# Optimization experiments

Hardware: AMD Instinct MI355X
Metric: run time of the kernel (lower is better)

Reference implementation:

```python
import math
import jax, jax.numpy as jnp
import numpy as np

B, T, D = 2048, 50, 256
NEG = -100000.0

def setup_inputs() -> dict:
    key = jax.random.key(0)
    ks = jax.random.split(key, 9)
    return {
        "x": jax.random.normal(ks[0], (B, T, D), dtype=jnp.float32),
        "mask": jax.random.randint(ks[1], (B, T, 1), 0, 2, dtype=jnp.int32),
        "time_decay": jax.random.uniform(ks[2], (B, T, 1), dtype=jnp.float32),
        "Wq": jax.random.normal(ks[3], (D, D), dtype=jnp.float32) * (1.0 / math.sqrt(D)),
        "bq": jax.random.normal(ks[4], (D,), dtype=jnp.float32) * 0.01,
        "Wk": jax.random.normal(ks[5], (D, D), dtype=jnp.float32) * (1.0 / math.sqrt(D)),
        "bk": jax.random.normal(ks[6], (D,), dtype=jnp.float32) * 0.01,
        "Wv": jax.random.normal(ks[7], (D, D), dtype=jnp.float32) * (1.0 / math.sqrt(D)),
        "bv": jax.random.normal(ks[8], (D,), dtype=jnp.float32) * 0.01,
    }

def reference(x, mask, time_decay, Wq, bq, Wk, bk, Wv, bv):
    # PositionalEncoding.forward: elementwise multiply by time-decay (broadcast over d_model)
    x = x * time_decay  # [B,T,D]
    q = jnp.einsum('btd,ed->bte', x, Wq) + bq
    k = jnp.einsum('btd,ed->bte', x, Wk) + bk
    v = jnp.einsum('btd,ed->bte', x, Wv) + bv
    # unusual Q/K-side masking (masked_fill before the matmul)
    keep = mask != 0  # [B,T,1]
    q = jnp.where(keep, q, NEG)
    k = jnp.where(keep, k, NEG)
    score = jnp.einsum('btd,bsd->bts', q, k) / math.sqrt(D)  # [B,T,T]
    score = jax.nn.softmax(score, axis=-1)
    # dropout is identity in eval mode
    out = jnp.einsum('bts,bsd->btd', score, v)  # [B,T,D]
    return out[:, -1, :]  # [B,D]
```

## Files before the change

### kernel.cpp

```cpp
#include <hip/hip_runtime.h>


namespace {
constexpr int kB = 2048;
constexpr int kT = 50;
constexpr int kD = 256;
constexpr double kNeg = -100000.0;
constexpr int oM2 = 0;
constexpr int oWvp = 65536;
constexpr int oV0 = 131072;
constexpr int oC = 131328;
constexpr int oW1 = 131584;
constexpr int oW2 = 131840;
constexpr int oDbl = 132096;
constexpr int kP = 257;
}

__global__ __launch_bounds__(256) void precomp(
    const float* __restrict__ Wq, const float* __restrict__ bq,
    const float* __restrict__ Wk, const float* __restrict__ bk,
    const float* __restrict__ Wv, float* __restrict__ ws) {
  const int t = threadIdx.x;
  const int wave = t >> 6;
  const int lane = t & 63;
  const int blk = blockIdx.x;
  __shared__ float coefL[kD];
  __shared__ double red[3][4];

  if (blk < 256) {
    const int a = blk;
    coefL[t] = Wq[(size_t)t * kD + a];
    __syncthreads();
    const float* kcol = Wk + t;
    float pre[8];
#pragma unroll
    for (int k = 0; k < 8; ++k) pre[k] = kcol[(size_t)k * kD];
    float acc = 0.f;
    for (int j0 = 0; j0 < kD; j0 += 8) {
      float cur[8];
#pragma unroll
      for (int k = 0; k < 8; ++k) cur[k] = pre[k];
      const int nx = (j0 + 8 < kD) ? (j0 + 8) : 0;
#pragma unroll
      for (int k = 0; k < 8; ++k) pre[k] = kcol[(size_t)(nx + k) * kD];
#pragma unroll
      for (int k = 0; k < 8; ++k) acc += coefL[j0 + k] * cur[k];
    }
    ws[oM2 + (a >> 2) * 1024 + 4 * t + (a & 3)] = acc;
  } else if (blk < 258) {
    const float* W = (blk == 256) ? Wk : Wq;
    const float* coef = (blk == 256) ? bq : bk;
    coefL[t] = coef[t];
    __syncthreads();
    const float* col = W + t;
    float pre[8];
#pragma unroll
    for (int k = 0; k < 8; ++k) pre[k] = col[(size_t)k * kD];
    double a0 = 0.0, a1 = 0.0;
    for (int j0 = 0; j0 < kD; j0 += 8) {
      float cur[8];
#pragma unroll
      for (int k = 0; k < 8; ++k) cur[k] = pre[k];
      const int nx = (j0 + 8 < kD) ? (j0 + 8) : 0;
#pragma unroll
      for (int k = 0; k < 8; ++k) pre[k] = col[(size_t)(nx + k) * kD];
#pragma unroll
      for (int k = 0; k < 8; ++k) {
        const double w = (double)cur[k];
        a0 += (double)coefL[j0 + k] * w;
        a1 += w;
      }
    }
    if (blk == 256) {
      ws[oV0 + t] = (float)a0;
      ws[oC + t] = (float)a1;
    } else {
      ws[oW1 + t] = (float)a0;
      ws[oW2 + t] = (float)a1;
      double p0 = (double)bk[t];
      double p1 = (double)bq[t] * (double)bk[t];
      double p2 = (double)bq[t];
#pragma unroll
      for (int off = 32; off; off >>= 1) {
        p0 += __shfl_xor(p0, off);
        p1 += __shfl_xor(p1, off);
        p2 += __shfl_xor(p2, off);
      }
      if (lane == 0) {
        red[0][wave] = p0;
        red[1][wave] = p1;
        red[2][wave] = p2;
      }
      __syncthreads();
      if (t == 0) {
        double* dcw = (double*)(ws + oDbl);
        dcw[0] = red[0][0] + red[0][1] + red[0][2] + red[0][3];
        dcw[1] = red[1][0] + red[1][1] + red[1][2] + red[1][3];
        dcw[2] = red[2][0] + red[2][1] + red[2][2] + red[2][3];
      }
    }
  } else {
    const int d4b = (blk - 258) * 4;
    float4 in[4];
#pragma unroll
    for (int k = 0; k < 4; ++k)
      in[k] = *(const float4*)(Wv + (size_t)t * kD + 4 * (d4b + k));
    float4* Wvp = (float4*)(ws + oWvp);
#pragma unroll
    for (int k = 0; k < 4; ++k) Wvp[(size_t)(d4b + k) * kD + t] = in[k];
  }
}

__global__ __launch_bounds__(512) void ukernel(
    const float* __restrict__ x, const float* __restrict__ td,
    const float* __restrict__ ws, float* __restrict__ uout) {
  const int tid = threadIdx.x;
  const int lane = tid & 63;
  const int w = tid >> 6;
  const int b0 = blockIdx.x * 4;
  __shared__ __align__(16) float xsL[4][kD];
  __shared__ __align__(16) float scr[2][4][kD];
  const float4* M2v = (const float4*)(ws + oM2);

  if (w < 4) {
    const int b = b0 + w;
    const float tdl = td[(size_t)b * kT + kT - 1];
    const float4 xv =
        ((const float4*)(x + ((size_t)b * kT + kT - 1) * kD))[lane];
    float4 xs;
    xs.x = xv.x * tdl; xs.y = xv.y * tdl;
    xs.z = xv.z * tdl; xs.w = xv.w * tdl;
    *(float4*)(&xsL[w][4 * lane]) = xs;
  }
  __syncthreads();

  {
    const int gU = w & 3;
    const int kh = w >> 2;
    const int col = 64 * gU + lane;
    const int kb = kh * 32;
    float4 A = M2v[(size_t)(kb + 0) * 256 + col];
    float4 B = M2v[(size_t)(kb + 1) * 256 + col];
    float4 C = M2v[(size_t)(kb + 2) * 256 + col];
    float4 D = M2v[(size_t)(kb + 3) * 256 + col];
    float acc[4] = {0.f, 0.f, 0.f, 0.f};
    for (int k4 = kb; k4 < kb + 32; k4 += 2) {
      const float4 c0 = A, c1 = B;
      A = C;
      B = D;
      const int n0 = (k4 + 4 < kb + 32) ? k4 + 4 : kb;
      const int n1 = (k4 + 5 < kb + 32) ? k4 + 5 : kb;
      C = M2v[(size_t)n0 * 256 + col];
      D = M2v[(size_t)n1 * 256 + col];
#pragma unroll
      for (int jb = 0; jb < 4; ++jb) {
        const float4 x0 = *(const float4*)(&xsL[jb][4 * k4]);
        const float4 x1 = *(const float4*)(&xsL[jb][4 * (k4 + 1)]);
        acc[jb] += x0.x * c0.x + x0.y * c0.y + x0.z * c0.z + x0.w * c0.w +
                   x1.x * c1.x + x1.y * c1.y + x1.z * c1.z + x1.w * c1.w;
      }
    }
#pragma unroll
    for (int jb = 0; jb < 4; ++jb) scr[kh][jb][col] = acc[jb];
  }
  __syncthreads();

#pragma unroll
  for (int rr = 0; rr < 2; ++rr) {
    const int idx = tid + rr * 512;
    const int mj = idx >> 8;
    const int mcol = idx & 255;
    uout[(size_t)(b0 + mj) * kD + mcol] =
        scr[0][mj][mcol] + scr[1][mj][mcol] + ws[oV0 + mcol];
  }
}

__global__ __launch_bounds__(256) void attnk(
    const float* __restrict__ x, const int* __restrict__ mask,
    const float* __restrict__ td, const float* __restrict__ ws,
    float* __restrict__ uy) {
  const int tid = threadIdx.x;
  const int lane = tid & 63;
  const int w = tid >> 6;
  const int b = blockIdx.x;
  __shared__ __align__(16) float xL[kT * kP + 4];
  __shared__ float vL[kD];
  __shared__ float pL[4][64];
  __shared__ float wL[64];

  const float* xb = x + (size_t)b * kT * kD;
  const int mqg = mask[(size_t)b * kT + (kT - 1)];

  {
    const float4* xv4 = (const float4*)xb;
#pragma unroll
    for (int k = 0; k < 13; ++k) {
      const int idx4 = tid + 256 * k;
      if (idx4 < kT * 64) {
        const int s = idx4 >> 6;
        const int d4 = idx4 & 63;
        const float4 v = xv4[idx4];
        float* dst = &xL[s * kP + 4 * d4];
        dst[0] = v.x; dst[1] = v.y; dst[2] = v.z; dst[3] = v.w;
      }
    }
    vL[tid] = mqg ? uy[(size_t)b * kD + tid] : ws[oC + tid];
  }

  const float mtd = (lane < kT) ? td[(size_t)b * kT + lane] : 0.f;
  const int mmk = (lane < kT) ? mask[(size_t)b * kT + lane] : 0;

  double Qb = 0.0, Sq = 0.0;
  if (w == 0) {
    const double* dc = (const double*)(ws + oDbl);
    const float tdl = __shfl(mtd, kT - 1);
    const float4 a1 = ((const float4*)(ws + oW1))[lane];
    const float4 a2 = ((const float4*)(ws + oW2))[lane];
    const float4 xv = ((const float4*)(xb + (size_t)(kT - 1) * kD))[lane];
    double s1 = (double)xv.x * a1.x + (double)xv.y * a1.y +
                (double)xv.z * a1.z + (double)xv.w * a1.w;
    double s2 = (double)xv.x * a2.x + (double)xv.y * a2.y +
                (double)xv.z * a2.z + (double)xv.w * a2.w;
#pragma unroll
    for (int off = 32; off; off >>= 1) {
      s1 += __shfl_xor(s1, off);
      s2 += __shfl_xor(s2, off);
    }
    Qb = (double)tdl * s1 + dc[1];
    Sq = (double)tdl * s2 + dc[2];
  }
  __syncthreads();

  {
    const int srow = (lane < kT) ? lane : 0;
    const float* xrow = &xL[srow * kP];
    const int dbase = 64 * w;
    float acc0 = 0.f, acc1 = 0.f;
#pragma unroll
    for (int t = 0; t < 64; t += 2) {
      acc0 += xrow[dbase + t] * vL[dbase + t];
      acc1 += xrow[dbase + t + 1] * vL[dbase + t + 1];
    }
    pL[w][lane] = acc0 + acc1;
  }
  __syncthreads();

  if (w == 0) {
    const double* dc = (const double*)(ws + oDbl);
    const float praw = pL[0][lane] + pL[1][lane] + pL[2][lane] + pL[3][lane];
    const float pfull = praw * mtd;
    const double Cm = kNeg * Sq * 0.0625;
    const double sbkd = dc[0];
    const double Cbb = 256.0 * 1.0e10 * 0.0625;
    double sc;
    if (lane < kT) {
      if (mqg)
        sc = mmk ? ((double)pfull + Qb) * 0.0625 : Cm;
      else
        sc = mmk ? kNeg * ((double)pfull + sbkd) * 0.0625 : Cbb;
    } else {
      sc = -1.0e300;
    }
    double m = sc;
#pragma unroll
    for (int off = 32; off; off >>= 1) {
      const double o = __shfl_xor(m, off);
      if (o > m) m = o;
    }
    const float e = __expf((float)(sc - m));
    float l = e;
#pragma unroll
    for (int off = 32; off; off >>= 1) l += __shfl_xor(l, off);
    wL[lane] = e * (1.0f / l) * mtd;
  }
  __syncthreads();

  {
    const int d = tid;
    float y0 = 0.f, y1 = 0.f;
#pragma unroll
    for (int s = 0; s < kT; s += 2) {
      y0 += wL[s] * xL[s * kP + d];
      y1 += wL[s + 1] * xL[(s + 1) * kP + d];
    }
    uy[(size_t)b * kD + d] = y0 + y1;
  }
}

__global__ __launch_bounds__(512) void okernel(
    const float* __restrict__ bv, const float* __restrict__ ws,
    float* __restrict__ io) {
  const int tid = threadIdx.x;
  const int lane = tid & 63;
  const int w = tid >> 6;
  const int b0 = blockIdx.x * 4;
  __shared__ __align__(16) float yL[4][kD];
  __shared__ __align__(16) float scr[2][4][kD];
  const float4* Wvv = (const float4*)(ws + oWvp);

#pragma unroll
  for (int rr = 0; rr < 2; ++rr) {
    const int idx = tid + rr * 512;
    const int mj = idx >> 8;
    const int mcol = idx & 255;
    yL[mj][mcol] = io[(size_t)(b0 + mj) * kD + mcol];
  }
  __syncthreads();

  {
    const int gU = w & 3;
    const int kh = w >> 2;
    const int col = 64 * gU + lane;
    const int kb = kh * 32;
    float4 A = Wvv[(size_t)(kb + 0) * 256 + col];
    float4 B = Wvv[(size_t)(kb + 1) * 256 + col];
    float4 C = Wvv[(size_t)(kb + 2) * 256 + col];
    float4 D = Wvv[(size_t)(kb + 3) * 256 + col];
    float acc[4] = {0.f, 0.f, 0.f, 0.f};
    for (int k4 = kb; k4 < kb + 32; k4 += 2) {
      const float4 c0 = A, c1 = B;
      A = C;
      B = D;
      const int n0 = (k4 + 4 < kb + 32) ? k4 + 4 : kb;
      const int n1 = (k4 + 5 < kb + 32) ? k4 + 5 : kb;
      C = Wvv[(size_t)n0 * 256 + col];
      D = Wvv[(size_t)n1 * 256 + col];
#pragma unroll
      for (int jb = 0; jb < 4; ++jb) {
        const float4 y0 = *(const float4*)(&yL[jb][4 * k4]);
        const float4 y1 = *(const float4*)(&yL[jb][4 * (k4 + 1)]);
        acc[jb] += y0.x * c0.x + y0.y * c0.y + y0.z * c0.z + y0.w * c0.w +
                   y1.x * c1.x + y1.y * c1.y + y1.z * c1.z + y1.w * c1.w;
      }
    }
#pragma unroll
    for (int jb = 0; jb < 4; ++jb) scr[kh][jb][col] = acc[jb];
  }
  __syncthreads();

#pragma unroll
  for (int rr = 0; rr < 2; ++rr) {
    const int idx = tid + rr * 512;
    const int mj = idx >> 8;
    const int mcol = idx & 255;
    io[(size_t)(b0 + mj) * kD + mcol] =
        scr[0][mj][mcol] + scr[1][mj][mcol] + bv[mcol];
  }
}

extern "C" void kernel_launch(void* const* d_in, const int* in_sizes, int n_in,
                              void* d_out, int out_size, void* d_ws,
                              size_t ws_size, hipStream_t stream) {
  const float* x = (const float*)d_in[0];
  const int* mask = (const int*)d_in[1];
  const float* td = (const float*)d_in[2];
  const float* Wq = (const float*)d_in[3];
  const float* bq = (const float*)d_in[4];
  const float* Wk = (const float*)d_in[5];
  const float* bk = (const float*)d_in[6];
  const float* Wv = (const float*)d_in[7];
  const float* bv = (const float*)d_in[8];
  float* ws = (float*)d_ws;
  float* out = (float*)d_out;
  (void)in_sizes; (void)n_in; (void)out_size; (void)ws_size;

  hipLaunchKernelGGL(precomp, dim3(274), dim3(256), 0, stream, Wq, bq, Wk, bk,
                     Wv, ws);
  hipLaunchKernelGGL(ukernel, dim3(kB / 4), dim3(512), 0, stream, x, td,
                     (const float*)ws, out);
  hipLaunchKernelGGL(attnk, dim3(kB), dim3(256), 0, stream, x, mask, td,
                     (const float*)ws, out);
  hipLaunchKernelGGL(okernel, dim3(kB / 4), dim3(512), 0, stream, bv,
                     (const float*)ws, out);
}
```

Before: 210.9 us.

## Fuse u-projection, attention and output projection into one per-batch kernel

Merges the three per-batch kernels (the u matvec, the attention, and the Wv output matvec) into a single kernel with one block per batch element. The u vector and the attention output y now stay in shared memory instead of round-tripping through global memory, and two launches are removed. In exchange, each 256-thread block reads the full 256x256 M2 and Wv matrices by itself, where previously each matrix read was shared across 4 batch rows. This raises L2 traffic and lowers per-block arithmetic intensity for the matvecs.

```diff
diff --git a/kernel.cpp b/kernel.cpp
--- a/kernel.cpp
+++ b/kernel.cpp
@@ -111,85 +111,24 @@
   }
 }
 
-__global__ __launch_bounds__(512) void ukernel(
-    const float* __restrict__ x, const float* __restrict__ td,
-    const float* __restrict__ ws, float* __restrict__ uout) {
-  const int tid = threadIdx.x;
-  const int lane = tid & 63;
-  const int w = tid >> 6;
-  const int b0 = blockIdx.x * 4;
-  __shared__ __align__(16) float xsL[4][kD];
-  __shared__ __align__(16) float scr[2][4][kD];
-  const float4* M2v = (const float4*)(ws + oM2);
-
-  if (w < 4) {
-    const int b = b0 + w;
-    const float tdl = td[(size_t)b * kT + kT - 1];
-    const float4 xv =
-        ((const float4*)(x + ((size_t)b * kT + kT - 1) * kD))[lane];
-    float4 xs;
-    xs.x = xv.x * tdl; xs.y = xv.y * tdl;
-    xs.z = xv.z * tdl; xs.w = xv.w * tdl;
-    *(float4*)(&xsL[w][4 * lane]) = xs;
-  }
-  __syncthreads();
-
-  {
-    const int gU = w & 3;
-    const int kh = w >> 2;
-    const int col = 64 * gU + lane;
-    const int kb = kh * 32;
-    float4 A = M2v[(size_t)(kb + 0) * 256 + col];
-    float4 B = M2v[(size_t)(kb + 1) * 256 + col];
-    float4 C = M2v[(size_t)(kb + 2) * 256 + col];
-    float4 D = M2v[(size_t)(kb + 3) * 256 + col];
-    float acc[4] = {0.f, 0.f, 0.f, 0.f};
-    for (int k4 = kb; k4 < kb + 32; k4 += 2) {
-      const float4 c0 = A, c1 = B;
-      A = C;
-      B = D;
-      const int n0 = (k4 + 4 < kb + 32) ? k4 + 4 : kb;
-      const int n1 = (k4 + 5 < kb + 32) ? k4 + 5 : kb;
-      C = M2v[(size_t)n0 * 256 + col];
-      D = M2v[(size_t)n1 * 256 + col];
-#pragma unroll
-      for (int jb = 0; jb < 4; ++jb) {
-        const float4 x0 = *(const float4*)(&xsL[jb][4 * k4]);
-        const float4 x1 = *(const float4*)(&xsL[jb][4 * (k4 + 1)]);
-        acc[jb] += x0.x * c0.x + x0.y * c0.y + x0.z * c0.z + x0.w * c0.w +
-                   x1.x * c1.x + x1.y * c1.y + x1.z * c1.z + x1.w * c1.w;
-      }
-    }
-#pragma unroll
-    for (int jb = 0; jb < 4; ++jb) scr[kh][jb][col] = acc[jb];
-  }
-  __syncthreads();
-
-#pragma unroll
-  for (int rr = 0; rr < 2; ++rr) {
-    const int idx = tid + rr * 512;
-    const int mj = idx >> 8;
-    const int mcol = idx & 255;
-    uout[(size_t)(b0 + mj) * kD + mcol] =
-        scr[0][mj][mcol] + scr[1][mj][mcol] + ws[oV0 + mcol];
-  }
-}
-
-__global__ __launch_bounds__(256) void attnk(
+__global__ __launch_bounds__(256) void fusedb(
     const float* __restrict__ x, const int* __restrict__ mask,
-    const float* __restrict__ td, const float* __restrict__ ws,
-    float* __restrict__ uy) {
+    const float* __restrict__ td, const float* __restrict__ bv,
+    const float* __restrict__ ws, float* __restrict__ out) {
   const int tid = threadIdx.x;
   const int lane = tid & 63;
   const int w = tid >> 6;
   const int b = blockIdx.x;
   __shared__ __align__(16) float xL[kT * kP + 4];
+  __shared__ __align__(16) float x49L[kD];
   __shared__ float vL[kD];
   __shared__ float pL[4][64];
   __shared__ float wL[64];
+  __shared__ __align__(16) float yL[kD];
 
   const float* xb = x + (size_t)b * kT * kD;
   const int mqg = mask[(size_t)b * kT + (kT - 1)];
+  const float td49 = td[(size_t)b * kT + kT - 1];
 
   {
     const float4* xv4 = (const float4*)xb;
@@ -204,7 +143,7 @@
         dst[0] = v.x; dst[1] = v.y; dst[2] = v.z; dst[3] = v.w;
       }
     }
-    vL[tid] = mqg ? uy[(size_t)b * kD + tid] : ws[oC + tid];
+    x49L[tid] = xb[(size_t)(kT - 1) * kD + tid];
   }
 
   const float mtd = (lane < kT) ? td[(size_t)b * kT + lane] : 0.f;
@@ -213,7 +152,6 @@
   double Qb = 0.0, Sq = 0.0;
   if (w == 0) {
     const double* dc = (const double*)(ws + oDbl);
-    const float tdl = __shfl(mtd, kT - 1);
     const float4 a1 = ((const float4*)(ws + oW1))[lane];
     const float4 a2 = ((const float4*)(ws + oW2))[lane];
     const float4 xv = ((const float4*)(xb + (size_t)(kT - 1) * kD))[lane];
@@ -226,8 +164,34 @@
       s1 += __shfl_xor(s1, off);
       s2 += __shfl_xor(s2, off);
     }
-    Qb = (double)tdl * s1 + dc[1];
-    Sq = (double)tdl * s2 + dc[2];
+    Qb = (double)td49 * s1 + dc[1];
+    Sq = (double)td49 * s2 + dc[2];
+  }
+  __syncthreads();
+
+  {
+    const int col = 64 * w + lane;
+    const float4* M2v = (const float4*)(ws + oM2);
+    float4 A = M2v[0 * 256 + col];
+    float4 B = M2v[1 * 256 + col];
+    float4 C = M2v[2 * 256 + col];
+    float4 D = M2v[3 * 256 + col];
+    float acc = 0.f;
+    for (int k4 = 0; k4 < 64; k4 += 2) {
+      const float4 c0 = A, c1 = B;
+      A = C;
+      B = D;
+      const int n0 = (k4 + 4 < 64) ? k4 + 4 : 0;
+      const int n1 = (k4 + 5 < 64) ? k4 + 5 : 1;
+      C = M2v[(size_t)n0 * 256 + col];
+      D = M2v[(size_t)n1 * 256 + col];
+      const float4 x0 = *(const float4*)(&x49L[4 * k4]);
+      const float4 x1 = *(const float4*)(&x49L[4 * (k4 + 1)]);
+      acc += x0.x * c0.x + x0.y * c0.y + x0.z * c0.z + x0.w * c0.w +
+             x1.x * c1.x + x1.y * c1.y + x1.z * c1.z + x1.w * c1.w;
+    }
+    const float u = td49 * acc + ws[oV0 + col];
+    vL[col] = mqg ? u : ws[oC + col];
   }
   __syncthreads();
 
@@ -283,68 +247,32 @@
       y0 += wL[s] * xL[s * kP + d];
       y1 += wL[s + 1] * xL[(s + 1) * kP + d];
     }
-    uy[(size_t)b * kD + d] = y0 + y1;
-  }
-}
-
-__global__ __launch_bounds__(512) void okernel(
-    const float* __restrict__ bv, const float* __restrict__ ws,
-    float* __restrict__ io) {
-  const int tid = threadIdx.x;
-  const int lane = tid & 63;
-  const int w = tid >> 6;
-  const int b0 = blockIdx.x * 4;
-  __shared__ __align__(16) float yL[4][kD];
-  __shared__ __align__(16) float scr[2][4][kD];
-  const float4* Wvv = (const float4*)(ws + oWvp);
-
-#pragma unroll
-  for (int rr = 0; rr < 2; ++rr) {
-    const int idx = tid + rr * 512;
-    const int mj = idx >> 8;
-    const int mcol = idx & 255;
-    yL[mj][mcol] = io[(size_t)(b0 + mj) * kD + mcol];
-  }
-  __syncthreads();
-
-  {
-    const int gU = w & 3;
-    const int kh = w >> 2;
-    const int col = 64 * gU + lane;
-    const int kb = kh * 32;
-    float4 A = Wvv[(size_t)(kb + 0) * 256 + col];
-    float4 B = Wvv[(size_t)(kb + 1) * 256 + col];
-    float4 C = Wvv[(size_t)(kb + 2) * 256 + col];
-    float4 D = Wvv[(size_t)(kb + 3) * 256 + col];
-    float acc[4] = {0.f, 0.f, 0.f, 0.f};
-    for (int k4 = kb; k4 < kb + 32; k4 += 2) {
+    yL[d] = y0 + y1;
+  }
+  __syncthreads();
+
+  {
+    const int col = 64 * w + lane;
+    const float4* Wvv = (const float4*)(ws + oWvp);
+    float4 A = Wvv[0 * 256 + col];
+    float4 B = Wvv[1 * 256 + col];
+    float4 C = Wvv[2 * 256 + col];
+    float4 D = Wvv[3 * 256 + col];
+    float acc = 0.f;
+    for (int k4 = 0; k4 < 64; k4 += 2) {
       const float4 c0 = A, c1 = B;
       A = C;
       B = D;
-      const int n0 = (k4 + 4 < kb + 32) ? k4 + 4 : kb;
-      const int n1 = (k4 + 5 < kb + 32) ? k4 + 5 : kb;
+      const int n0 = (k4 + 4 < 64) ? k4 + 4 : 0;
+      const int n1 = (k4 + 5 < 64) ? k4 + 5 : 1;
       C = Wvv[(size_t)n0 * 256 + col];
       D = Wvv[(size_t)n1 * 256 + col];
-#pragma unroll
-      for (int jb = 0; jb < 4; ++jb) {
-        const float4 y0 = *(const float4*)(&yL[jb][4 * k4]);
-        const float4 y1 = *(const float4*)(&yL[jb][4 * (k4 + 1)]);
-        acc[jb] += y0.x * c0.x + y0.y * c0.y + y0.z * c0.z + y0.w * c0.w +
-                   y1.x * c1.x + y1.y * c1.y + y1.z * c1.z + y1.w * c1.w;
-      }
-    }
-#pragma unroll
-    for (int jb = 0; jb < 4; ++jb) scr[kh][jb][col] = acc[jb];
-  }
-  __syncthreads();
-
-#pragma unroll
-  for (int rr = 0; rr < 2; ++rr) {
-    const int idx = tid + rr * 512;
-    const int mj = idx >> 8;
-    const int mcol = idx & 255;
-    io[(size_t)(b0 + mj) * kD + mcol] =
-        scr[0][mj][mcol] + scr[1][mj][mcol] + bv[mcol];
+      const float4 y0 = *(const float4*)(&yL[4 * k4]);
+      const float4 y1 = *(const float4*)(&yL[4 * (k4 + 1)]);
+      acc += y0.x * c0.x + y0.y * c0.y + y0.z * c0.z + y0.w * c0.w +
+             y1.x * c1.x + y1.y * c1.y + y1.z * c1.z + y1.w * c1.w;
+    }
+    out[(size_t)b * kD + col] = acc + bv[col];
   }
 }
 
@@ -366,10 +294,6 @@
 
   hipLaunchKernelGGL(precomp, dim3(274), dim3(256), 0, stream, Wq, bq, Wk, bk,
                      Wv, ws);
-  hipLaunchKernelGGL(ukernel, dim3(kB / 4), dim3(512), 0, stream, x, td,
+  hipLaunchKernelGGL(fusedb, dim3(kB), dim3(256), 0, stream, x, mask, td, bv,
                      (const float*)ws, out);
-  hipLaunchKernelGGL(attnk, dim3(kB), dim3(256), 0, stream, x, mask, td,
-                     (const float*)ws, out);
-  hipLaunchKernelGGL(okernel, dim3(kB / 4), dim3(512), 0, stream, bv,
-                     (const float*)ws, out);
-}
+}
```

Result: slower. 225.2 us (+6.8%).
